# Kernel optimization log

Measured on AMD Instinct MI355X. Metric: run time of the kernel, lower is better.

## Reference

```python
import jax, jax.numpy as jnp
import numpy as np

DIM = 512
HEADS = 8


def setup_inputs() -> dict:
    key = jax.random.key(0)
    k1, k2, k3 = jax.random.split(key, 3)
    x = jax.random.normal(k1, (4, DIM, 64, 64), dtype=jnp.float32)
    # kaiming_normal fan_out, linear: std = 1/sqrt(fan_out)
    w_qkv = jax.random.normal(k2, (3 * DIM, DIM), dtype=jnp.float32) / np.sqrt(3 * DIM)
    b_qkv = jnp.zeros((3 * DIM,), dtype=jnp.float32)
    w_proj = jax.random.normal(k3, (DIM, DIM), dtype=jnp.float32) / np.sqrt(DIM)
    b_proj = jnp.zeros((DIM,), dtype=jnp.float32)
    return {"x": x, "w_qkv": w_qkv, "b_qkv": b_qkv, "w_proj": w_proj, "b_proj": b_proj}


def reference(x, w_qkv, b_qkv, w_proj, b_proj):
    B, C, H, W = x.shape
    N = H * W
    hd = C // HEADS
    scale = hd ** -0.5
    x_flat = x.reshape(B, C, N).transpose(0, 2, 1)          # [B, N, C]
    qkv = x_flat @ w_qkv.T + b_qkv                           # [B, N, 3C]
    q, k, v = jnp.split(qkv, 3, axis=-1)
    q = q.reshape(B, N, HEADS, hd).transpose(0, 2, 1, 3)     # [B, h, N, d]
    k = k.reshape(B, N, HEADS, hd).transpose(0, 2, 1, 3)
    v = v.reshape(B, N, HEADS, hd).transpose(0, 2, 1, 3)
    attn = jnp.einsum('bhnd,bhmd->bhnm', q, k) * scale       # [B, h, N, N]
    attn = jnp.clip(attn, -10.0, 10.0)
    attn = jax.nn.softmax(attn, axis=-1)
    out = jnp.einsum('bhnm,bhmd->bhnd', attn, v)             # [B, h, N, d]
    out = out.transpose(0, 2, 1, 3).reshape(B, N, C)         # [B, N, C]
    out = out @ w_proj.T + b_proj
    out = out.transpose(0, 2, 1).reshape(B, C, H, W)
    return x + out
```

## Files before the change

### kernel.cpp

```cpp
#include <hip/hip_runtime.h>

typedef float f32x4 __attribute__((ext_vector_type(4)));
typedef __bf16 bf16x8 __attribute__((ext_vector_type(8)));
typedef unsigned short u16;
typedef unsigned int u32;
typedef u16 u16x4 __attribute__((ext_vector_type(4)));
typedef u16 u16x8 __attribute__((ext_vector_type(8)));

#define DEV static __device__ __forceinline__

constexpr int B = 4, C = 512, NH = 8, HD = 64, NN = 4096, C3 = 1536;
constexpr float K_PRESCALE = 0.125f * 1.4426950408889634f;
constexpr float CLIP2 = 10.0f * 1.4426950408889634f;

DEV u16 f2bf(float f) { union { __bf16 b; u16 s; } u; u.b = (__bf16)f; return u.s; }

#if __has_builtin(__builtin_amdgcn_exp2f)
DEV float fast_exp2(float x) { return __builtin_amdgcn_exp2f(x); }
#else
DEV float fast_exp2(float x) { return __expf(x * 0.6931471805599453f); }
#endif

#if __has_builtin(__builtin_amdgcn_fmed3f)
DEV float clamp2(float x) { return __builtin_amdgcn_fmed3f(x, -CLIP2, CLIP2); }
#else
DEV float clamp2(float x) { return fminf(fmaxf(x, -CLIP2), CLIP2); }
#endif

__global__ __launch_bounds__(256) void k_transpose(const float* __restrict__ x,
                                                   u16* __restrict__ Xt) {
  __shared__ float tile[64][65];
  const int n0 = blockIdx.x * 64, c0 = blockIdx.y * 64, b = blockIdx.z;
  const int t = threadIdx.x;
  const int cl = t >> 4, n4 = (t & 15) * 4;
#pragma unroll
  for (int rep = 0; rep < 4; ++rep) {
    const int c = rep * 16 + cl;
    const f32x4 v = *(const f32x4*)(x + ((size_t)(b * C + c0 + c)) * NN + n0 + n4);
#pragma unroll
    for (int j = 0; j < 4; ++j) tile[c][n4 + j] = v[j];
  }
  __syncthreads();
#pragma unroll
  for (int rep = 0; rep < 16; ++rep) {
    const int n = rep * 4 + (t >> 6);
    const int c = t & 63;
    Xt[((size_t)(b * NN + n0 + n)) * C + c0 + c] = f2bf(tile[c][n]);
  }
}

__global__ __launch_bounds__(256) void k_cvtw(const float* __restrict__ wq,
                                              const float* __restrict__ wp,
                                              u16* __restrict__ Wq, u16* __restrict__ Wp) {
  const int idx = blockIdx.x * 256 + threadIdx.x;
  const int NQ = C3 * C / 4;
  const float* src;
  u16* dst;
  int i4;
  if (idx < NQ) { src = wq; dst = Wq; i4 = idx; }
  else          { src = wp; dst = Wp; i4 = idx - NQ; }
  const f32x4 v = *(const f32x4*)(src + (size_t)i4 * 4);
  u16x4 o;
#pragma unroll
  for (int j = 0; j < 4; ++j) o[j] = f2bf(v[j]);
  *(u16x4*)(dst + (size_t)i4 * 4) = o;
}

__global__ __launch_bounds__(256) void k_qkv(const u16* __restrict__ Xt,
                                             const u16* __restrict__ W,
                                             const float* __restrict__ bias,
                                             u16* __restrict__ Q, u16* __restrict__ Kq,
                                             u16* __restrict__ Vt) {
  __shared__ u16 smem[16384];
  u16* Alds = smem;
  u16* Blds = smem + 8192;
  const int nt = blockIdx.x, mt = blockIdx.y, b = blockIdx.z;
  const int t = threadIdx.x, w = t >> 6, l = t & 63;
  const int l15 = l & 15, l4 = l >> 4;
  const int wr = w >> 1, wc = w & 1;
  f32x4 acc[4][4] = {};
  const u16* Abase = Xt + (size_t)(b * NN + nt * 128) * C;
  const u16* Bbase = W + (size_t)(mt * 128) * C;

  for (int kt = 0; kt < C / 64; ++kt) {
    __syncthreads();
#pragma unroll
    for (int i = 0; i < 4; ++i) {
      const int cch = t + 256 * i;
      const int r = cch >> 3, kb = (cch & 7) * 16;
      const int sw = kb ^ ((r & 7) << 4);
      *(f32x4*)((char*)Alds + r * 128 + sw) =
          *(const f32x4*)((const char*)(Abase + (size_t)r * C + kt * 64) + kb);
      *(f32x4*)((char*)Blds + r * 128 + sw) =
          *(const f32x4*)((const char*)(Bbase + (size_t)r * C + kt * 64) + kb);
    }
    __syncthreads();
#pragma unroll
    for (int ks = 0; ks < 2; ++ks) {
      bf16x8 af[4], bfr[4];
#pragma unroll
      for (int ri = 0; ri < 4; ++ri) {
        const int row = wr * 64 + ri * 16 + l15;
        af[ri] = *(const bf16x8*)((const char*)Alds + row * 128 +
                                  ((ks * 64 + l4 * 16) ^ ((row & 7) << 4)));
      }
#pragma unroll
      for (int cj = 0; cj < 4; ++cj) {
        const int row = wc * 64 + cj * 16 + l15;
        bfr[cj] = *(const bf16x8*)((const char*)Blds + row * 128 +
                                   ((ks * 64 + l4 * 16) ^ ((row & 7) << 4)));
      }
#pragma unroll
      for (int ri = 0; ri < 4; ++ri)
#pragma unroll
        for (int cj = 0; cj < 4; ++cj)
          acc[ri][cj] = __builtin_amdgcn_mfma_f32_16x16x32_bf16(af[ri], bfr[cj], acc[ri][cj], 0, 0, 0);
    }
  }

  __syncthreads();
  const int sec = mt >> 2;
  const int mtl = mt & 3;
  if (sec < 2) {
#pragma unroll
    for (int ri = 0; ri < 4; ++ri)
#pragma unroll
      for (int cj = 0; cj < 4; ++cj) {
        const int m_l = wc * 64 + cj * 16 + l15;
        const float bv = bias[mt * 128 + m_l];
        const float sc = (sec == 1) ? K_PRESCALE : 1.0f;
#pragma unroll
        for (int r = 0; r < 4; ++r) {
          const int n_l = wr * 64 + ri * 16 + l4 * 4 + r;
          *(u16*)((char*)smem + n_l * 256 + ((m_l * 2) ^ ((n_l & 7) << 4))) =
              f2bf((acc[ri][cj][r] + bv) * sc);
        }
      }
    __syncthreads();
    u16* dst = (sec == 0) ? Q : Kq;
#pragma unroll
    for (int rep = 0; rep < 8; ++rep) {
      const int idx = rep * 256 + t;
      const int n_l = idx >> 4, ch = idx & 15;
      const u16x8 v = *(const u16x8*)((char*)smem + n_l * 256 + ((ch * 16) ^ ((n_l & 7) << 4)));
      const int hh = mtl * 2 + (ch >> 3), dd = (ch & 7) * 8;
      *(u16x8*)(dst + ((size_t)(b * NH + hh) * NN + nt * 128 + n_l) * HD + dd) = v;
    }
  } else {
#pragma unroll
    for (int ri = 0; ri < 4; ++ri)
#pragma unroll
      for (int cj = 0; cj < 4; ++cj) {
        const int m_l = wc * 64 + cj * 16 + l15;
        const float bv = bias[mt * 128 + m_l];
        const int nb = wr * 64 + ri * 16 + l4 * 4;
        u16x4 pv;
#pragma unroll
        for (int r = 0; r < 4; ++r) pv[r] = f2bf(acc[ri][cj][r] + bv);
        *(u16x4*)((char*)smem + m_l * 256 + ((nb * 2) ^ ((m_l & 7) << 4))) = pv;
      }
    __syncthreads();
#pragma unroll
    for (int rep = 0; rep < 8; ++rep) {
      const int idx = rep * 256 + t;
      const int m_l = idx >> 4, ch = idx & 15;
      const u16x8 v = *(const u16x8*)((char*)smem + m_l * 256 + ((ch * 16) ^ ((m_l & 7) << 4)));
      const int hh = mtl * 2 + (m_l >> 6), dd = m_l & 63;
      *(u16x8*)(Vt + ((size_t)(b * NH + hh) * HD + dd) * NN + nt * 128 + ch * 8) = v;
    }
  }
}

__global__ __launch_bounds__(256) void k_attn(const u16* __restrict__ Q,
                                              const u16* __restrict__ K,
                                              const u16* __restrict__ Vt,
                                              u16* __restrict__ AO) {
  __shared__ u16 Klds[4096];
  __shared__ u16 Vlds[4096];
  __shared__ u16 Plds[4096];
  const int qt = blockIdx.x, h = blockIdx.y, b = blockIdx.z;
  const int bh = b * NH + h;
  const int t = threadIdx.x, w = t >> 6, l = t & 63;
  const int l15 = l & 15, l4 = l >> 4;
  const int q0 = qt * 64;

  const u16* qb = Q + ((size_t)bh * NN + q0 + w * 16 + l15) * HD + l4 * 8;
  bf16x8 qf[2];
  qf[0] = *(const bf16x8*)(qb);
  qf[1] = *(const bf16x8*)(qb + 32);

  union { u16 s; __bf16 b; } ob;
  ob.s = 0x3F80;
  bf16x8 ones;
#pragma unroll
  for (int j = 0; j < 8; ++j) ones[j] = ob.b;

  f32x4 o[4] = {};
  f32x4 rsa = {};

  const int sr = t >> 3, scb = (t & 7) * 16;
  const int ssw = scb ^ ((sr & 7) << 4);
  char* kwp = (char*)Klds + sr * 128 + ssw;
  char* vwp = (char*)Vlds + sr * 128 + ssw;
  const char* kg = (const char*)(K + (size_t)bh * NN * HD) + sr * 128 + scb;
  const char* vg = (const char*)(Vt + (size_t)bh * HD * NN) + (size_t)sr * 8192 + scb;

  const int sw7 = (l15 & 7) << 4;

  f32x4 kr0 = *(const f32x4*)kg;
  f32x4 kr1 = *(const f32x4*)(kg + 4096);
  f32x4 vr0 = *(const f32x4*)vg;
  f32x4 vr1 = *(const f32x4*)(vg + (size_t)32 * 8192);
  *(f32x4*)kwp = kr0;
  *(f32x4*)(kwp + 4096) = kr1;
  *(f32x4*)vwp = vr0;
  *(f32x4*)(vwp + 4096) = vr1;
  __syncthreads();

  constexpr int NT = NN / 64;
  for (int kv = 0; kv < NT; ++kv) {
    if (kv + 1 < NT) {
      kg += 8192;
      vg += 128;
      kr0 = *(const f32x4*)kg;
      kr1 = *(const f32x4*)(kg + 4096);
      vr0 = *(const f32x4*)vg;
      vr1 = *(const f32x4*)(vg + (size_t)32 * 8192);
    }

    f32x4 s[4] = {};
#pragma unroll
    for (int ks = 0; ks < 2; ++ks) {
#pragma unroll
      for (int cj = 0; cj < 4; ++cj) {
        const bf16x8 kf = *(const bf16x8*)((const char*)Klds + (cj * 16 + l15) * 128 +
                                           ((ks * 64 + l4 * 16) ^ sw7));
        s[cj] = __builtin_amdgcn_mfma_f32_16x16x32_bf16(qf[ks], kf, s[cj], 0, 0, 0);
      }
    }
#pragma unroll
    for (int cj = 0; cj < 4; ++cj) {
      const int colb = (cj * 16 + l15) * 2;
#pragma unroll
      for (int r = 0; r < 4; ++r) {
        const float p = fast_exp2(clamp2(s[cj][r]));
        const int row = w * 16 + l4 * 4 + r;
        *(u16*)((char*)Plds + row * 128 + (colb ^ ((row & 7) << 4))) = f2bf(p);
      }
    }
    __syncthreads();

#pragma unroll
    for (int ks = 0; ks < 2; ++ks) {
      const int prow = w * 16 + l15;
      const bf16x8 pa = *(const bf16x8*)((const char*)Plds + prow * 128 +
                                         ((ks * 64 + l4 * 16) ^ sw7));
#pragma unroll
      for (int cj = 0; cj < 4; ++cj) {
        const bf16x8 vf = *(const bf16x8*)((const char*)Vlds + (cj * 16 + l15) * 128 +
                                           ((ks * 64 + l4 * 16) ^ sw7));
        o[cj] = __builtin_amdgcn_mfma_f32_16x16x32_bf16(pa, vf, o[cj], 0, 0, 0);
      }
      rsa = __builtin_amdgcn_mfma_f32_16x16x32_bf16(pa, ones, rsa, 0, 0, 0);
    }
    __syncthreads();

    if (kv + 1 < NT) {
      *(f32x4*)kwp = kr0;
      *(f32x4*)(kwp + 4096) = kr1;
      *(f32x4*)vwp = vr0;
      *(f32x4*)(vwp + 4096) = vr1;
    }
    __syncthreads();
  }

  float inv[4];
#pragma unroll
  for (int r = 0; r < 4; ++r) inv[r] = 1.0f / rsa[r];
#pragma unroll
  for (int cj = 0; cj < 4; ++cj)
#pragma unroll
    for (int r = 0; r < 4; ++r) {
      const int n = q0 + w * 16 + l4 * 4 + r;
      const int c = h * 64 + cj * 16 + l15;
      AO[((size_t)(b * NN + n)) * C + c] = f2bf(o[cj][r] * inv[r]);
    }
}

__global__ __launch_bounds__(256) void k_proj(const u16* __restrict__ AO,
                                              const u16* __restrict__ Wp,
                                              const float* __restrict__ bias,
                                              const float* __restrict__ x,
                                              float* __restrict__ out) {
  __shared__ u16 smem[16384];
  u16* Alds = smem;
  u16* Blds = smem + 8192;
  const int nt = blockIdx.x, ct = blockIdx.y, b = blockIdx.z;
  const int t = threadIdx.x, w = t >> 6, l = t & 63;
  const int l15 = l & 15, l4 = l >> 4;
  const int wr = w >> 1, wc = w & 1;
  f32x4 acc[4][4] = {};
  const u16* Abase = AO + (size_t)(b * NN + nt * 128) * C;
  const u16* Bbase = Wp + (size_t)(ct * 128) * C;

  for (int kt = 0; kt < C / 64; ++kt) {
    __syncthreads();
#pragma unroll
    for (int i = 0; i < 4; ++i) {
      const int cch = t + 256 * i;
      const int r = cch >> 3, kb = (cch & 7) * 16;
      const int sw = kb ^ ((r & 7) << 4);
      *(f32x4*)((char*)Alds + r * 128 + sw) =
          *(const f32x4*)((const char*)(Abase + (size_t)r * C + kt * 64) + kb);
      *(f32x4*)((char*)Blds + r * 128 + sw) =
          *(const f32x4*)((const char*)(Bbase + (size_t)r * C + kt * 64) + kb);
    }
    __syncthreads();
#pragma unroll
    for (int ks = 0; ks < 2; ++ks) {
      bf16x8 af[4], bfr[4];
#pragma unroll
      for (int ri = 0; ri < 4; ++ri) {
        const int row = wr * 64 + ri * 16 + l15;
        af[ri] = *(const bf16x8*)((const char*)Alds + row * 128 +
                                  ((ks * 64 + l4 * 16) ^ ((row & 7) << 4)));
      }
#pragma unroll
      for (int cj = 0; cj < 4; ++cj) {
        const int row = wc * 64 + cj * 16 + l15;
        bfr[cj] = *(const bf16x8*)((const char*)Blds + row * 128 +
                                   ((ks * 64 + l4 * 16) ^ ((row & 7) << 4)));
      }
#pragma unroll
      for (int ri = 0; ri < 4; ++ri)
#pragma unroll
        for (int cj = 0; cj < 4; ++cj)
          acc[ri][cj] = __builtin_amdgcn_mfma_f32_16x16x32_bf16(af[ri], bfr[cj], acc[ri][cj], 0, 0, 0);
    }
  }

  float* fs = (float*)smem;
  __syncthreads();
#pragma unroll
  for (int p = 0; p < 2; ++p) {
    if (p) __syncthreads();
    if (wc == p) {
#pragma unroll
      for (int ri = 0; ri < 4; ++ri)
#pragma unroll
        for (int cj = 0; cj < 4; ++cj) {
          const int co = cj * 16 + l15;
          const float bv = bias[ct * 128 + p * 64 + co];
          const int nb = wr * 64 + ri * 16 + l4 * 4;
          f32x4 vv;
#pragma unroll
          for (int r = 0; r < 4; ++r) vv[r] = acc[ri][cj][r] + bv;
          *(f32x4*)((char*)fs + co * 512 + ((nb * 4) ^ ((co & 7) << 4))) = vv;
        }
    }
    __syncthreads();
#pragma unroll
    for (int rep = 0; rep < 8; ++rep) {
      const int idx = rep * 256 + t;
      const int co = idx >> 5, ch = idx & 31;
      f32x4 vv = *(const f32x4*)((char*)fs + co * 512 + ((ch * 16) ^ ((co & 7) << 4)));
      const size_t base = ((size_t)(b * C + ct * 128 + p * 64 + co)) * NN + nt * 128 + ch * 4;
      const f32x4 xr = *(const f32x4*)(x + base);
#pragma unroll
      for (int r = 0; r < 4; ++r) vv[r] += xr[r];
      *(f32x4*)(out + base) = vv;
    }
  }
}

extern "C" void kernel_launch(void* const* d_in, const int* in_sizes, int n_in,
                              void* d_out, int out_size, void* d_ws, size_t ws_size,
                              hipStream_t stream) {
  const float* x      = (const float*)d_in[0];
  const float* w_qkv  = (const float*)d_in[1];
  const float* b_qkv  = (const float*)d_in[2];
  const float* w_proj = (const float*)d_in[3];
  const float* b_proj = (const float*)d_in[4];
  float* out = (float*)d_out;
  char* ws = (char*)d_ws;

  const size_t SZ_XT = (size_t)B * NN * C * 2;
  const size_t SZ_WQ = (size_t)C3 * C * 2;
  const size_t SZ_WP = (size_t)C * C * 2;
  const size_t SZ_QK = (size_t)B * NH * NN * HD * 2;

  u16* Xt = (u16*)(ws);
  u16* Wq = (u16*)(ws + SZ_XT);
  u16* Wp = (u16*)(ws + SZ_XT + SZ_WQ);
  u16* Qb = (u16*)(ws + SZ_XT + SZ_WQ + SZ_WP);
  u16* Kb = (u16*)(ws + SZ_XT + SZ_WQ + SZ_WP + SZ_QK);
  u16* Vt = (u16*)(ws + SZ_XT + SZ_WQ + SZ_WP + 2 * SZ_QK);
  u16* AO = Xt;

  k_transpose<<<dim3(NN / 64, C / 64, B), 256, 0, stream>>>(x, Xt);
  k_cvtw<<<dim3((C3 * C + C * C) / 4 / 256), 256, 0, stream>>>(w_qkv, w_proj, Wq, Wp);
  k_qkv<<<dim3(NN / 128, C3 / 128, B), 256, 0, stream>>>(Xt, Wq, b_qkv, Qb, Kb, Vt);
  k_attn<<<dim3(NN / 64, NH, B), 256, 0, stream>>>(Qb, Kb, Vt, AO);
  k_proj<<<dim3(NN / 128, C / 128, B), 256, 0, stream>>>(AO, Wp, b_proj, x, out);
}
```

Before: 369.6 us.

## Double-buffer K/V tiles in LDS and drop extra barriers in attention loop

Splits the K and V shared-memory tiles into two buffers, so the next tile's prefetched registers are written into the alternate buffer while the current one is still being read. This cuts the per-iteration barriers from three to one. The barrier between writing P and reading it is also removed, since each wave writes and reads only its own P rows. The cost is more LDS per block (two extra 8 KB tiles), which may reduce how many blocks fit on a compute unit.

```diff
diff --git a/kernel.cpp b/kernel.cpp
--- a/kernel.cpp
+++ b/kernel.cpp
@@ -175,8 +175,8 @@
                                               const u16* __restrict__ K,
                                               const u16* __restrict__ Vt,
                                               u16* __restrict__ AO) {
-  __shared__ u16 Klds[4096];
-  __shared__ u16 Vlds[4096];
+  __shared__ u16 Klds[2][4096];
+  __shared__ u16 Vlds[2][4096];
   __shared__ u16 Plds[4096];
   const int qt = blockIdx.x, h = blockIdx.y, b = blockIdx.z;
   const int bh = b * NH + h;
@@ -199,27 +199,30 @@
   f32x4 rsa = {};
 
   const int sr = t >> 3, scb = (t & 7) * 16;
-  const int ssw = scb ^ ((sr & 7) << 4);
-  char* kwp = (char*)Klds + sr * 128 + ssw;
-  char* vwp = (char*)Vlds + sr * 128 + ssw;
+  const int swoff = (scb ^ ((sr & 7) << 4)) + sr * 128;
   const char* kg = (const char*)(K + (size_t)bh * NN * HD) + sr * 128 + scb;
   const char* vg = (const char*)(Vt + (size_t)bh * HD * NN) + (size_t)sr * 8192 + scb;
 
   const int sw7 = (l15 & 7) << 4;
 
-  f32x4 kr0 = *(const f32x4*)kg;
-  f32x4 kr1 = *(const f32x4*)(kg + 4096);
-  f32x4 vr0 = *(const f32x4*)vg;
-  f32x4 vr1 = *(const f32x4*)(vg + (size_t)32 * 8192);
-  *(f32x4*)kwp = kr0;
-  *(f32x4*)(kwp + 4096) = kr1;
-  *(f32x4*)vwp = vr0;
-  *(f32x4*)(vwp + 4096) = vr1;
+  {
+    const f32x4 a0 = *(const f32x4*)kg;
+    const f32x4 a1 = *(const f32x4*)(kg + 4096);
+    const f32x4 a2 = *(const f32x4*)vg;
+    const f32x4 a3 = *(const f32x4*)(vg + (size_t)32 * 8192);
+    *(f32x4*)((char*)Klds + swoff) = a0;
+    *(f32x4*)((char*)Klds + swoff + 4096) = a1;
+    *(f32x4*)((char*)Vlds + swoff) = a2;
+    *(f32x4*)((char*)Vlds + swoff + 4096) = a3;
+  }
   __syncthreads();
 
   constexpr int NT = NN / 64;
+  f32x4 kr0, kr1, vr0, vr1;
   for (int kv = 0; kv < NT; ++kv) {
-    if (kv + 1 < NT) {
+    const int cur = kv & 1;
+    const bool more = (kv + 1 < NT);
+    if (more) {
       kg += 8192;
       vg += 128;
       kr0 = *(const f32x4*)kg;
@@ -227,13 +230,15 @@
       vr0 = *(const f32x4*)vg;
       vr1 = *(const f32x4*)(vg + (size_t)32 * 8192);
     }
+    const char* kbase = (const char*)Klds + cur * 8192;
+    const char* vbase = (const char*)Vlds + cur * 8192;
 
     f32x4 s[4] = {};
 #pragma unroll
     for (int ks = 0; ks < 2; ++ks) {
 #pragma unroll
       for (int cj = 0; cj < 4; ++cj) {
-        const bf16x8 kf = *(const bf16x8*)((const char*)Klds + (cj * 16 + l15) * 128 +
+        const bf16x8 kf = *(const bf16x8*)(kbase + (cj * 16 + l15) * 128 +
                                            ((ks * 64 + l4 * 16) ^ sw7));
         s[cj] = __builtin_amdgcn_mfma_f32_16x16x32_bf16(qf[ks], kf, s[cj], 0, 0, 0);
       }
@@ -248,7 +253,6 @@
         *(u16*)((char*)Plds + row * 128 + (colb ^ ((row & 7) << 4))) = f2bf(p);
       }
     }
-    __syncthreads();
 
 #pragma unroll
     for (int ks = 0; ks < 2; ++ks) {
@@ -257,19 +261,20 @@
                                          ((ks * 64 + l4 * 16) ^ sw7));
 #pragma unroll
       for (int cj = 0; cj < 4; ++cj) {
-        const bf16x8 vf = *(const bf16x8*)((const char*)Vlds + (cj * 16 + l15) * 128 +
+        const bf16x8 vf = *(const bf16x8*)(vbase + (cj * 16 + l15) * 128 +
                                            ((ks * 64 + l4 * 16) ^ sw7));
         o[cj] = __builtin_amdgcn_mfma_f32_16x16x32_bf16(pa, vf, o[cj], 0, 0, 0);
       }
       rsa = __builtin_amdgcn_mfma_f32_16x16x32_bf16(pa, ones, rsa, 0, 0, 0);
     }
-    __syncthreads();
-
-    if (kv + 1 < NT) {
-      *(f32x4*)kwp = kr0;
-      *(f32x4*)(kwp + 4096) = kr1;
-      *(f32x4*)vwp = vr0;
-      *(f32x4*)(vwp + 4096) = vr1;
+
+    if (more) {
+      char* kw = (char*)Klds + (cur ^ 1) * 8192 + swoff;
+      char* vw = (char*)Vlds + (cur ^ 1) * 8192 + swoff;
+      *(f32x4*)kw = kr0;
+      *(f32x4*)(kw + 4096) = kr1;
+      *(f32x4*)vw = vr0;
+      *(f32x4*)(vw + 4096) = vr1;
     }
     __syncthreads();
   }
```

Measured after the change: 385.2 us. 1.04x slower.

## Load GEMM tiles via global_load_lds and drop a barrier in attention

Applied to the files above, without the earlier changes.

The QKV and projection GEMMs now copy their A and B tiles straight from global memory into LDS with the global_load_lds builtin when the compiler supports it. The source address is swizzled so the LDS layout stays the same, and the copy no longer passes through registers or separate LDS store instructions. The attention kernel also loses the barrier between writing P tiles to LDS and reading them back. Each wave reads only its own 16 P rows, so the barrier is assumed unneeded. That relies on intra-wave ordering of LDS accesses, and the direct-to-LDS copy relies on the existing barrier (which may not emit vmcnt waits) to make the data visible before use.

```diff
diff --git a/kernel.cpp b/kernel.cpp
--- a/kernel.cpp
+++ b/kernel.cpp
@@ -25,6 +25,17 @@
 DEV float clamp2(float x) { return __builtin_amdgcn_fmed3f(x, -CLIP2, CLIP2); }
 #else
 DEV float clamp2(float x) { return fminf(fmaxf(x, -CLIP2), CLIP2); }
+#endif
+
+#if __has_builtin(__builtin_amdgcn_global_load_lds)
+#define HAVE_GLL 1
+DEV void gll16(const void* g, void* l) {
+  __builtin_amdgcn_global_load_lds(
+      (const __attribute__((address_space(1))) void*)g,
+      (__attribute__((address_space(3))) void*)l, 16, 0, 0);
+}
+#else
+#define HAVE_GLL 0
 #endif
 
 __global__ __launch_bounds__(256) void k_transpose(const float* __restrict__ x,
@@ -84,6 +95,16 @@
 
   for (int kt = 0; kt < C / 64; ++kt) {
     __syncthreads();
+#if HAVE_GLL
+#pragma unroll
+    for (int i = 0; i < 4; ++i) {
+      const int cch = t + 256 * i;
+      const int r = cch >> 3;
+      const int sc = ((cch & 7) * 16) ^ ((r & 7) << 4);
+      gll16((const char*)(Abase + (size_t)r * C + kt * 64) + sc, (char*)Alds + cch * 16);
+      gll16((const char*)(Bbase + (size_t)r * C + kt * 64) + sc, (char*)Blds + cch * 16);
+    }
+#else
 #pragma unroll
     for (int i = 0; i < 4; ++i) {
       const int cch = t + 256 * i;
@@ -94,6 +115,7 @@
       *(f32x4*)((char*)Blds + r * 128 + sw) =
           *(const f32x4*)((const char*)(Bbase + (size_t)r * C + kt * 64) + kb);
     }
+#endif
     __syncthreads();
 #pragma unroll
     for (int ks = 0; ks < 2; ++ks) {
@@ -248,7 +270,6 @@
         *(u16*)((char*)Plds + row * 128 + (colb ^ ((row & 7) << 4))) = f2bf(p);
       }
     }
-    __syncthreads();
 
 #pragma unroll
     for (int ks = 0; ks < 2; ++ks) {
@@ -305,6 +326,16 @@
 
   for (int kt = 0; kt < C / 64; ++kt) {
     __syncthreads();
+#if HAVE_GLL
+#pragma unroll
+    for (int i = 0; i < 4; ++i) {
+      const int cch = t + 256 * i;
+      const int r = cch >> 3;
+      const int sc = ((cch & 7) * 16) ^ ((r & 7) << 4);
+      gll16((const char*)(Abase + (size_t)r * C + kt * 64) + sc, (char*)Alds + cch * 16);
+      gll16((const char*)(Bbase + (size_t)r * C + kt * 64) + sc, (char*)Blds + cch * 16);
+    }
+#else
 #pragma unroll
     for (int i = 0; i < 4; ++i) {
       const int cch = t + 256 * i;
@@ -315,6 +346,7 @@
       *(f32x4*)((char*)Blds + r * 128 + sw) =
           *(const f32x4*)((const char*)(Bbase + (size_t)r * C + kt * 64) + kb);
     }
+#endif
     __syncthreads();
 #pragma unroll
     for (int ks = 0; ks < 2; ++ks) {
```

New measurement: 378.7 us. 2.4% more time.
